# Optimization experiments

Measured on AMD Instinct MI355X. Metric: run time of the kernel, lower is better.

## Reference

```python
import jax, jax.numpy as jnp
import numpy as np

EMB = 768
HEADS = 12


def setup_inputs() -> dict:
    key = jax.random.key(0)
    ks = jax.random.split(key, 5)
    B, T, C = 4, 2048, EMB
    scale = 0.02
    return {
        "x": jax.random.normal(ks[0], (B, T, C), dtype=jnp.float32),
        "w_qkv": jax.random.normal(ks[1], (C, 3 * C), dtype=jnp.float32) * scale,
        "b_qkv": jnp.zeros((3 * C,), dtype=jnp.float32),
        "w_proj": jax.random.normal(ks[2], (C, C), dtype=jnp.float32) * scale,
        "b_proj": jnp.zeros((C,), dtype=jnp.float32),
    }


def reference(x, w_qkv, b_qkv, w_proj, b_proj):
    B, T, C = x.shape
    H = HEADS
    Dh = C // H
    qkv = x @ w_qkv + b_qkv  # [B,T,3C]
    q, k, v = jnp.split(qkv, 3, axis=-1)
    # [B,H,T,Dh]
    q = q.reshape(B, T, H, Dh).transpose(0, 2, 1, 3)
    k = k.reshape(B, T, H, Dh).transpose(0, 2, 1, 3)
    v = v.reshape(B, T, H, Dh).transpose(0, 2, 1, 3)
    scores = jnp.einsum("bhqd,bhkd->bhqk", q, k) / jnp.sqrt(jnp.float32(Dh))
    causal = jnp.tril(jnp.ones((T, T), dtype=bool))  # [T,T]
    scores = jnp.where(causal, scores, jnp.float32(-jnp.inf))
    attn = jax.nn.softmax(scores, axis=-1)
    y = jnp.einsum("bhqk,bhkd->bhqd", attn, v)  # [B,H,T,Dh]
    y = y.transpose(0, 2, 1, 3).reshape(B, T, C)
    return y @ w_proj + b_proj
```

## Files before the change

### kernel.cpp

```cpp
#include <hip/hip_runtime.h>

typedef __attribute__((ext_vector_type(8))) short short8;
typedef __attribute__((ext_vector_type(4))) float f32x4;
typedef __attribute__((ext_vector_type(4))) unsigned short ushort4v;
typedef unsigned short ushort;

__device__ __forceinline__ ushort f2bf(float f) {
    union { float f; unsigned u; } v; v.f = f;
    unsigned r = v.u + 0x7fff + ((v.u >> 16) & 1);
    return (ushort)(r >> 16);
}

__device__ __forceinline__ unsigned pkbf(float lo, float hi) {
    unsigned r;
    asm("v_cvt_pk_bf16_f32 %0, %1, %2" : "=v"(r) : "v"(lo), "v"(hi));
    return r;
}

__device__ __forceinline__ short8 bfscale8(short8 v, float s) {
    short8 o;
#pragma unroll
    for (int j = 0; j < 8; j++) {
        union { float f; unsigned u; } t; t.u = ((unsigned)(ushort)v[j]) << 16;
        o[j] = (short)f2bf(t.f * s);
    }
    return o;
}

__device__ __forceinline__ void gload16(const void* g, void* l) {
    __builtin_amdgcn_global_load_lds(
        (const __attribute__((address_space(1))) void*)g,
        (__attribute__((address_space(3))) void*)l, 16, 0, 0);
}

__global__ __launch_bounds__(256) void cvt_kernel(const float* __restrict__ in,
                                                  ushort* __restrict__ out, int n4) {
    int i = blockIdx.x * 256 + threadIdx.x;
    if (i < n4) {
        float4 v = ((const float4*)in)[i];
        ushort4v o;
        o.x = f2bf(v.x); o.y = f2bf(v.y); o.z = f2bf(v.z); o.w = f2bf(v.w);
        ((ushort4v*)out)[i] = o;
    }
}

__global__ __launch_bounds__(256) void tcvt_kernel(const float* __restrict__ in,
                                                   ushort* __restrict__ out, int R, int C0) {
    __shared__ float tile[32][33];
    const int tx = threadIdx.x & 31, ty = threadIdx.x >> 5;
    const int bx = blockIdx.x, by = blockIdx.y;
#pragma unroll
    for (int j = ty; j < 32; j += 8)
        tile[j][tx] = in[(size_t)(by * 32 + j) * C0 + bx * 32 + tx];
    __syncthreads();
#pragma unroll
    for (int j = ty; j < 32; j += 8)
        out[(size_t)(bx * 32 + j) * R + by * 32 + tx] = f2bf(tile[tx][j]);
}

__global__ __launch_bounds__(256) void vtrans_kernel(const ushort* __restrict__ qkv,
                                                     ushort* __restrict__ vt) {
    constexpr int T = 2048, H = 12, CC = 2304;
    const int bh = blockIdx.z;
    const int b = bh / H, h = bh - b * H;
    const int t0 = blockIdx.x * 32, d0 = blockIdx.y * 32;
    __shared__ ushort tile[32][33];
    const int tx = threadIdx.x & 31, ty = threadIdx.x >> 5;
#pragma unroll
    for (int j = ty; j < 32; j += 8)
        tile[j][tx] = qkv[(size_t)(b * T + t0 + j) * CC + 1536 + h * 64 + d0 + tx];
    __syncthreads();
#pragma unroll
    for (int j = ty; j < 32; j += 8)
        vt[((size_t)bh * 64 + d0 + j) * T + t0 + tx] = tile[tx][j];
}

template <bool OUT_F32>
__global__ __launch_bounds__(256)
void gemm128(const ushort* __restrict__ A, const ushort* __restrict__ Bt,
             const float* __restrict__ bias, void* __restrict__ Cout,
             int M, int N, int K) {
    __shared__ __attribute__((aligned(16))) ushort sA[2][128 * 32];
    __shared__ __attribute__((aligned(16))) ushort sB[2][128 * 32];
    const int tid = threadIdx.x;
    const int lane = tid & 63, w = tid >> 6;
    const int wm = w >> 1, wn = w & 1;
    const int c = lane & 15, g = lane >> 4;
    const int m0 = blockIdx.x * 128, n0 = blockIdx.y * 128;

    const f32x4 fz = {0.f, 0.f, 0.f, 0.f};
    f32x4 acc[4][4];
#pragma unroll
    for (int i = 0; i < 4; i++)
#pragma unroll
        for (int j = 0; j < 4; j++) acc[i][j] = fz;

    const int e0 = tid * 8, e1 = (256 + tid) * 8;
    const ushort* Ab0 = A + (size_t)(m0 + (e0 >> 5)) * K + (e0 & 31);
    const ushort* Ab1 = A + (size_t)(m0 + (e1 >> 5)) * K + (e1 & 31);
    const ushort* Bb0 = Bt + (size_t)(n0 + (e0 >> 5)) * K + (e0 & 31);
    const ushort* Bb1 = Bt + (size_t)(n0 + (e1 >> 5)) * K + (e1 & 31);

#define GSTAGE(buf, kt)                                   \
    do {                                                  \
        gload16(Ab0 + (kt) * 32, &sA[buf][e0]);           \
        gload16(Ab1 + (kt) * 32, &sA[buf][e1]);           \
        gload16(Bb0 + (kt) * 32, &sB[buf][e0]);           \
        gload16(Bb1 + (kt) * 32, &sB[buf][e1]);           \
    } while (0)

    const int nk = K >> 5;
    GSTAGE(0, 0);
    for (int kt = 0; kt < nk; ++kt) {
        __syncthreads();
        if (kt + 1 < nk) GSTAGE((kt + 1) & 1, kt + 1);
        const int cb = kt & 1;
        short8 af[4], bfr[4];
#pragma unroll
        for (int mi = 0; mi < 4; mi++)
            af[mi] = *(const short8*)&sA[cb][(wm * 64 + mi * 16 + c) * 32 + g * 8];
#pragma unroll
        for (int ni = 0; ni < 4; ni++)
            bfr[ni] = *(const short8*)&sB[cb][(wn * 64 + ni * 16 + c) * 32 + g * 8];
#pragma unroll
        for (int mi = 0; mi < 4; mi++)
#pragma unroll
            for (int ni = 0; ni < 4; ni++)
                acc[mi][ni] = __builtin_amdgcn_mfma_f32_16x16x32_bf16(
                    af[mi], bfr[ni], acc[mi][ni], 0, 0, 0);
    }
#undef GSTAGE

    const int crow = m0 + wm * 64, ccol = n0 + wn * 64;
#pragma unroll
    for (int ni = 0; ni < 4; ni++) {
        const float bv = bias[ccol + ni * 16 + c];
#pragma unroll
        for (int mi = 0; mi < 4; mi++) {
#pragma unroll
            for (int r = 0; r < 4; r++) {
                float v = acc[mi][ni][r] + bv;
                size_t idx = (size_t)(crow + mi * 16 + g * 4 + r) * N + ccol + ni * 16 + c;
                if (OUT_F32) ((float*)Cout)[idx] = v;
                else ((ushort*)Cout)[idx] = f2bf(v);
            }
        }
    }
}

__global__ __launch_bounds__(256)
void attn_fwd(const ushort* __restrict__ qkv, const ushort* __restrict__ vt,
              ushort* __restrict__ outp) {
    constexpr int T = 2048, H = 12, CC = 2304;
    const int bh = blockIdx.y;
    const int b = bh / H, h = bh - b * H;
    const int p = blockIdx.x;
    const int qt_hi = 31 - p, qt_lo = p;
    const int tid = threadIdx.x;
    const int w = tid >> 6, lane = tid & 63;
    const int c = lane & 15, g = lane >> 4;

    __shared__ __attribute__((aligned(16))) ushort sK[2][64 * 64];
    __shared__ __attribute__((aligned(16))) ushort sV[2][64 * 64];

    const int qb[2] = {qt_hi * 64 + w * 16, qt_lo * 64 + w * 16};
    const int qtl[2] = {qt_hi, qt_lo};

    const float SCL = 0.125f * 1.44269504f;
    short8 qf0[2], qf1[2];
#pragma unroll
    for (int ss = 0; ss < 2; ++ss) {
        const ushort* qp = qkv + (size_t)(b * T + qb[ss] + c) * CC + h * 64 + g * 8;
        qf0[ss] = bfscale8(*(const short8*)qp, SCL);
        qf1[ss] = bfscale8(*(const short8*)(qp + 32), SCL);
    }

    const f32x4 fz = {0.f, 0.f, 0.f, 0.f};
    f32x4 accO[2][4];
    f32x4 accL[2];
#pragma unroll
    for (int ss = 0; ss < 2; ++ss) {
        accL[ss] = fz;
#pragma unroll
        for (int ni = 0; ni < 4; ni++) accO[ss][ni] = fz;
    }

    short8 onesf;
    {
        ushort ov = (c == 0) ? (ushort)0x3F80 : (ushort)0;
#pragma unroll
        for (int j = 0; j < 8; j++) onesf[j] = (short)ov;
    }

    const int a_ = c >> 2, r_ = c & 3;
    const int rowE = 8 * a_ + r_ + 4 * (a_ & 1);
    const int rowO = 8 * a_ + r_ + 4 * ((a_ & 1) ^ 1);
    const int kaE0 = rowE * 64 + ((g ^ (rowE & 7)) << 3);
    const int kaE1 = rowE * 64 + (((4 + g) ^ (rowE & 7)) << 3);
    const int kaO0 = rowO * 64 + ((g ^ (rowO & 7)) << 3);
    const int kaO1 = rowO * 64 + (((4 + g) ^ (rowO & 7)) << 3);

    const int rowA = w * 8 + (lane >> 3);
    const int rowB = 32 + rowA;
    const int ps0 = lane & 7;
    const ushort* kS0 = qkv + (size_t)(b * T + rowA) * CC + 768 + h * 64 + ((ps0 ^ (rowA & 7)) << 3);
    const ushort* kS1 = qkv + (size_t)(b * T + rowB) * CC + 768 + h * 64 + ((ps0 ^ (rowB & 7)) << 3);
    const ushort* vS0 = vt + ((size_t)bh * 64 + rowA) * T + ((ps0 ^ (rowA & 7)) << 3);
    const ushort* vS1 = vt + ((size_t)bh * 64 + rowB) * T + ((ps0 ^ (rowB & 7)) << 3);
    const int ldK0 = (w * 8) * 64 + lane * 8;
    const int ldK1 = (32 + w * 8) * 64 + lane * 8;

#define ASTAGE(buf, kv0)                                                         \
    do {                                                                         \
        gload16(kS0 + (size_t)(kv0)*CC, &sK[buf][ldK0]);                         \
        gload16(kS1 + (size_t)(kv0)*CC, &sK[buf][ldK1]);                         \
        gload16(vS0 + (kv0), &sV[buf][ldK0]);                                    \
        gload16(vS1 + (kv0), &sV[buf][ldK1]);                                    \
    } while (0)

    ASTAGE(0, 0);
    int cur = 0;

    union U8 { unsigned u[4]; short8 s; };

    for (int t = 0; t <= qt_hi; ++t) {
        __syncthreads();
        if (t < qt_hi) ASTAGE(cur ^ 1, (t + 1) * 64);
        const ushort* K_ = &sK[cur][0];
        const ushort* V_ = &sV[cur][0];
        const bool both = (t <= qt_lo);

        f32x4 sc[2][4];
#pragma unroll
        for (int ni = 0; ni < 4; ni++) { sc[0][ni] = fz; sc[1][ni] = fz; }
#pragma unroll
        for (int ni = 0; ni < 4; ++ni) {
            const int off = (ni >> 1) * 2048;
            const int a0 = (ni & 1) ? kaO0 : kaE0;
            const int a1 = (ni & 1) ? kaO1 : kaE1;
            short8 kf0 = *(const short8*)&K_[off + a0];
            short8 kf1 = *(const short8*)&K_[off + a1];
            sc[0][ni] = __builtin_amdgcn_mfma_f32_16x16x32_bf16(kf0, qf0[0], sc[0][ni], 0, 0, 0);
            sc[0][ni] = __builtin_amdgcn_mfma_f32_16x16x32_bf16(kf1, qf1[0], sc[0][ni], 0, 0, 0);
            if (both) {
                sc[1][ni] = __builtin_amdgcn_mfma_f32_16x16x32_bf16(kf0, qf0[1], sc[1][ni], 0, 0, 0);
                sc[1][ni] = __builtin_amdgcn_mfma_f32_16x16x32_bf16(kf1, qf1[1], sc[1][ni], 0, 0, 0);
            }
        }

#pragma unroll
        for (int ss = 0; ss < 2; ++ss) {
            if (ss == 1 && !both) continue;
            if (t == qtl[ss]) {
                const int qg = qb[ss] + c;
#pragma unroll
                for (int ni = 0; ni < 4; ++ni) {
                    const int kvb = t * 64 + 8 * g + 4 * ((g & 1) ^ (ni & 1)) + 32 * (ni >> 1);
#pragma unroll
                    for (int r = 0; r < 4; ++r)
                        sc[ss][ni][r] = (kvb + r > qg) ? -1e30f : sc[ss][ni][r];
                }
            }
#pragma unroll
            for (int ni = 0; ni < 4; ++ni)
#pragma unroll
                for (int r = 0; r < 4; ++r)
                    sc[ss][ni][r] = __builtin_amdgcn_exp2f(sc[ss][ni][r]);
        }

        const bool godd = (g & 1);
#pragma unroll
        for (int ks = 0; ks < 2; ++ks) {
            short8 pf0, pf1;
            {
                f32x4 pa = godd ? sc[0][2 * ks + 1] : sc[0][2 * ks];
                f32x4 pb = godd ? sc[0][2 * ks] : sc[0][2 * ks + 1];
                U8 u;
                u.u[0] = pkbf(pa[0], pa[1]); u.u[1] = pkbf(pa[2], pa[3]);
                u.u[2] = pkbf(pb[0], pb[1]); u.u[3] = pkbf(pb[2], pb[3]);
                pf0 = u.s;
            }
            if (both) {
                f32x4 pa = godd ? sc[1][2 * ks + 1] : sc[1][2 * ks];
                f32x4 pb = godd ? sc[1][2 * ks] : sc[1][2 * ks + 1];
                U8 u;
                u.u[0] = pkbf(pa[0], pa[1]); u.u[1] = pkbf(pa[2], pa[3]);
                u.u[2] = pkbf(pb[0], pb[1]); u.u[3] = pkbf(pb[2], pb[3]);
                pf1 = u.s;
            }
#pragma unroll
            for (int ni = 0; ni < 4; ++ni) {
                short8 vf = *(const short8*)&V_[(ni * 16 + c) * 64 + (((ks * 4 + g) ^ (c & 7)) << 3)];
                accO[0][ni] = __builtin_amdgcn_mfma_f32_16x16x32_bf16(pf0, vf, accO[0][ni], 0, 0, 0);
                if (both)
                    accO[1][ni] = __builtin_amdgcn_mfma_f32_16x16x32_bf16(pf1, vf, accO[1][ni], 0, 0, 0);
            }
            accL[0] = __builtin_amdgcn_mfma_f32_16x16x32_bf16(pf0, onesf, accL[0], 0, 0, 0);
            if (both)
                accL[1] = __builtin_amdgcn_mfma_f32_16x16x32_bf16(pf1, onesf, accL[1], 0, 0, 0);
        }
        cur ^= 1;
    }
#undef ASTAGE

#pragma unroll
    for (int ss = 0; ss < 2; ++ss) {
        float linv[4];
#pragma unroll
        for (int r = 0; r < 4; r++) {
            float lv = __shfl(accL[ss][r], lane & 48, 64);
            linv[r] = 1.0f / lv;
        }
#pragma unroll
        for (int ni = 0; ni < 4; ni++)
#pragma unroll
            for (int r = 0; r < 4; r++) {
                float v = accO[ss][ni][r] * linv[r];
                outp[(size_t)(b * T + qb[ss] + g * 4 + r) * 768 + h * 64 + ni * 16 + c] = f2bf(v);
            }
    }
}

extern "C" void kernel_launch(void* const* d_in, const int* in_sizes, int n_in,
                              void* d_out, int out_size, void* d_ws, size_t ws_size,
                              hipStream_t stream) {
    const float* x      = (const float*)d_in[0];
    const float* w_qkv  = (const float*)d_in[1];
    const float* b_qkv  = (const float*)d_in[2];
    const float* w_proj = (const float*)d_in[3];
    const float* b_proj = (const float*)d_in[4];
    float* out = (float*)d_out;

    constexpr int B = 4, T = 2048, C = 768, H = 12;
    constexpr int M = B * T;
    constexpr int N1 = 3 * C;

    char* ws = (char*)d_ws;
    ushort* xb      = (ushort*)(ws);
    ushort* wqkvT   = (ushort*)(ws + 12582912);
    ushort* wprojT  = (ushort*)(ws + 16121856);
    ushort* qkvb    = (ushort*)(ws + 17301504);
    ushort* vtb     = (ushort*)(ws + 55050240);
    ushort* attnout = (ushort*)(ws + 67633152);

    cvt_kernel<<<(M * C / 4 + 255) / 256, 256, 0, stream>>>(x, xb, M * C / 4);
    tcvt_kernel<<<dim3(N1 / 32, C / 32), 256, 0, stream>>>(w_qkv, wqkvT, C, N1);
    tcvt_kernel<<<dim3(C / 32, C / 32), 256, 0, stream>>>(w_proj, wprojT, C, C);
    gemm128<false><<<dim3(M / 128, N1 / 128), 256, 0, stream>>>(xb, wqkvT, b_qkv, qkvb, M, N1, C);
    vtrans_kernel<<<dim3(T / 32, 2, B * H), 256, 0, stream>>>(qkvb, vtb);
    attn_fwd<<<dim3(16, B * H), 256, 0, stream>>>(qkvb, vtb, attnout);
    gemm128<true><<<dim3(M / 128, C / 128), 256, 0, stream>>>(attnout, wprojT, b_proj, out, M, C, C);
}
```

Measured before the change: 219.1 us.

## Fuse prep kernels, write V transposed from QKV GEMM, triple-buffer attention loads

Merges the x conversion and both weight transpose-conversions into one launch, and removes the separate V-transpose kernel by having the QKV GEMM epilogue write V columns directly into the transposed layout. The attention kernel moves from double to triple buffering of K/V tiles, using explicit vmcnt waits and raw barriers so loads run two tiles ahead, and raises wave priority around MFMA blocks. This cuts launch overhead and an extra pass over V, at the cost of more LDS per block and strided 8-byte stores in the GEMM epilogue.

```diff
diff --git a/kernel.cpp b/kernel.cpp
--- a/kernel.cpp
+++ b/kernel.cpp
@@ -33,22 +33,29 @@
         (__attribute__((address_space(3))) void*)l, 16, 0, 0);
 }
 
-__global__ __launch_bounds__(256) void cvt_kernel(const float* __restrict__ in,
-                                                  ushort* __restrict__ out, int n4) {
-    int i = blockIdx.x * 256 + threadIdx.x;
-    if (i < n4) {
-        float4 v = ((const float4*)in)[i];
+__global__ __launch_bounds__(256)
+void prep_kernel(const float* __restrict__ x, ushort* __restrict__ xb,
+                 const float* __restrict__ wq, ushort* __restrict__ wqT,
+                 const float* __restrict__ wp, ushort* __restrict__ wpT) {
+    __shared__ float tile[32][33];
+    const int bid = blockIdx.x;
+    if (bid < 6144) {
+        int i = bid * 256 + threadIdx.x;
+        float4 v = ((const float4*)x)[i];
         ushort4v o;
         o.x = f2bf(v.x); o.y = f2bf(v.y); o.z = f2bf(v.z); o.w = f2bf(v.w);
-        ((ushort4v*)out)[i] = o;
-    }
-}
-
-__global__ __launch_bounds__(256) void tcvt_kernel(const float* __restrict__ in,
-                                                   ushort* __restrict__ out, int R, int C0) {
-    __shared__ float tile[32][33];
+        ((ushort4v*)xb)[i] = o;
+        return;
+    }
+    const float* in; ushort* out; int R, C0, bx, by;
+    if (bid < 6144 + 1728) {
+        const int idx = bid - 6144;
+        in = wq; out = wqT; R = 768; C0 = 2304; bx = idx % 72; by = idx / 72;
+    } else {
+        const int idx = bid - 7872;
+        in = wp; out = wpT; R = 768; C0 = 768; bx = idx % 24; by = idx / 24;
+    }
     const int tx = threadIdx.x & 31, ty = threadIdx.x >> 5;
-    const int bx = blockIdx.x, by = blockIdx.y;
 #pragma unroll
     for (int j = ty; j < 32; j += 8)
         tile[j][tx] = in[(size_t)(by * 32 + j) * C0 + bx * 32 + tx];
@@ -58,28 +65,11 @@
         out[(size_t)(bx * 32 + j) * R + by * 32 + tx] = f2bf(tile[tx][j]);
 }
 
-__global__ __launch_bounds__(256) void vtrans_kernel(const ushort* __restrict__ qkv,
-                                                     ushort* __restrict__ vt) {
-    constexpr int T = 2048, H = 12, CC = 2304;
-    const int bh = blockIdx.z;
-    const int b = bh / H, h = bh - b * H;
-    const int t0 = blockIdx.x * 32, d0 = blockIdx.y * 32;
-    __shared__ ushort tile[32][33];
-    const int tx = threadIdx.x & 31, ty = threadIdx.x >> 5;
-#pragma unroll
-    for (int j = ty; j < 32; j += 8)
-        tile[j][tx] = qkv[(size_t)(b * T + t0 + j) * CC + 1536 + h * 64 + d0 + tx];
-    __syncthreads();
-#pragma unroll
-    for (int j = ty; j < 32; j += 8)
-        vt[((size_t)bh * 64 + d0 + j) * T + t0 + tx] = tile[tx][j];
-}
-
-template <bool OUT_F32>
+template <bool OUT_F32, bool WRITE_VT>
 __global__ __launch_bounds__(256)
 void gemm128(const ushort* __restrict__ A, const ushort* __restrict__ Bt,
              const float* __restrict__ bias, void* __restrict__ Cout,
-             int M, int N, int K) {
+             ushort* __restrict__ vt, int M, int N, int K) {
     __shared__ __attribute__((aligned(16))) ushort sA[2][128 * 32];
     __shared__ __attribute__((aligned(16))) ushort sB[2][128 * 32];
     const int tid = threadIdx.x;
@@ -135,14 +125,31 @@
 #pragma unroll
     for (int ni = 0; ni < 4; ni++) {
         const float bv = bias[ccol + ni * 16 + c];
-#pragma unroll
-        for (int mi = 0; mi < 4; mi++) {
-#pragma unroll
-            for (int r = 0; r < 4; r++) {
-                float v = acc[mi][ni][r] + bv;
-                size_t idx = (size_t)(crow + mi * 16 + g * 4 + r) * N + ccol + ni * 16 + c;
-                if (OUT_F32) ((float*)Cout)[idx] = v;
-                else ((ushort*)Cout)[idx] = f2bf(v);
+        if (WRITE_VT && (ccol + ni * 16) >= 1536) {
+            const int col = ccol + ni * 16 + c;
+            const int hv = (col - 1536) >> 6;
+            const int dv = (col - 1536) & 63;
+#pragma unroll
+            for (int mi = 0; mi < 4; mi++) {
+                const int row0 = crow + mi * 16 + g * 4;
+                const int bidx = row0 >> 11, tt = row0 & 2047;
+                ushort4v o;
+                o.x = f2bf(acc[mi][ni][0] + bv);
+                o.y = f2bf(acc[mi][ni][1] + bv);
+                o.z = f2bf(acc[mi][ni][2] + bv);
+                o.w = f2bf(acc[mi][ni][3] + bv);
+                *(ushort4v*)&vt[((size_t)(bidx * 12 + hv) * 64 + dv) * 2048 + tt] = o;
+            }
+        } else {
+#pragma unroll
+            for (int mi = 0; mi < 4; mi++) {
+#pragma unroll
+                for (int r = 0; r < 4; r++) {
+                    float v = acc[mi][ni][r] + bv;
+                    size_t idx = (size_t)(crow + mi * 16 + g * 4 + r) * N + ccol + ni * 16 + c;
+                    if (OUT_F32) ((float*)Cout)[idx] = v;
+                    else ((ushort*)Cout)[idx] = f2bf(v);
+                }
             }
         }
     }
@@ -160,8 +167,8 @@
     const int w = tid >> 6, lane = tid & 63;
     const int c = lane & 15, g = lane >> 4;
 
-    __shared__ __attribute__((aligned(16))) ushort sK[2][64 * 64];
-    __shared__ __attribute__((aligned(16))) ushort sV[2][64 * 64];
+    __shared__ __attribute__((aligned(16))) ushort sK[3][64 * 64];
+    __shared__ __attribute__((aligned(16))) ushort sV[3][64 * 64];
 
     const int qb[2] = {qt_hi * 64 + w * 16, qt_lo * 64 + w * 16};
     const int qtl[2] = {qt_hi, qt_lo};
@@ -219,13 +226,19 @@
     } while (0)
 
     ASTAGE(0, 0);
-    int cur = 0;
+    ASTAGE(1, 64);
+    int cur = 0, pfb = 2;
 
     union U8 { unsigned u[4]; short8 s; };
 
     for (int t = 0; t <= qt_hi; ++t) {
-        __syncthreads();
-        if (t < qt_hi) ASTAGE(cur ^ 1, (t + 1) * 64);
+        if (t + 1 <= qt_hi) asm volatile("s_waitcnt vmcnt(4)" ::: "memory");
+        else                asm volatile("s_waitcnt vmcnt(0)" ::: "memory");
+        __builtin_amdgcn_s_barrier();
+        asm volatile("" ::: "memory");
+        __builtin_amdgcn_sched_barrier(0);
+        if (t + 2 <= qt_hi) ASTAGE(pfb, (t + 2) * 64);
+
         const ushort* K_ = &sK[cur][0];
         const ushort* V_ = &sV[cur][0];
         const bool both = (t <= qt_lo);
@@ -233,6 +246,7 @@
         f32x4 sc[2][4];
 #pragma unroll
         for (int ni = 0; ni < 4; ni++) { sc[0][ni] = fz; sc[1][ni] = fz; }
+        __builtin_amdgcn_s_setprio(1);
 #pragma unroll
         for (int ni = 0; ni < 4; ++ni) {
             const int off = (ni >> 1) * 2048;
@@ -247,6 +261,7 @@
                 sc[1][ni] = __builtin_amdgcn_mfma_f32_16x16x32_bf16(kf1, qf1[1], sc[1][ni], 0, 0, 0);
             }
         }
+        __builtin_amdgcn_s_setprio(0);
 
 #pragma unroll
         for (int ss = 0; ss < 2; ++ss) {
@@ -288,6 +303,7 @@
                 u.u[2] = pkbf(pb[0], pb[1]); u.u[3] = pkbf(pb[2], pb[3]);
                 pf1 = u.s;
             }
+            __builtin_amdgcn_s_setprio(1);
 #pragma unroll
             for (int ni = 0; ni < 4; ++ni) {
                 short8 vf = *(const short8*)&V_[(ni * 16 + c) * 64 + (((ks * 4 + g) ^ (c & 7)) << 3)];
@@ -298,8 +314,10 @@
             accL[0] = __builtin_amdgcn_mfma_f32_16x16x32_bf16(pf0, onesf, accL[0], 0, 0, 0);
             if (both)
                 accL[1] = __builtin_amdgcn_mfma_f32_16x16x32_bf16(pf1, onesf, accL[1], 0, 0, 0);
-        }
-        cur ^= 1;
+            __builtin_amdgcn_s_setprio(0);
+        }
+        cur = (cur == 2) ? 0 : cur + 1;
+        pfb = (pfb == 2) ? 0 : pfb + 1;
     }
 #undef ASTAGE
 
@@ -343,11 +361,10 @@
     ushort* vtb     = (ushort*)(ws + 55050240);
     ushort* attnout = (ushort*)(ws + 67633152);
 
-    cvt_kernel<<<(M * C / 4 + 255) / 256, 256, 0, stream>>>(x, xb, M * C / 4);
-    tcvt_kernel<<<dim3(N1 / 32, C / 32), 256, 0, stream>>>(w_qkv, wqkvT, C, N1);
-    tcvt_kernel<<<dim3(C / 32, C / 32), 256, 0, stream>>>(w_proj, wprojT, C, C);
-    gemm128<false><<<dim3(M / 128, N1 / 128), 256, 0, stream>>>(xb, wqkvT, b_qkv, qkvb, M, N1, C);
-    vtrans_kernel<<<dim3(T / 32, 2, B * H), 256, 0, stream>>>(qkvb, vtb);
+    prep_kernel<<<8448, 256, 0, stream>>>(x, xb, w_qkv, wqkvT, w_proj, wprojT);
+    gemm128<false, true><<<dim3(M / 128, N1 / 128), 256, 0, stream>>>(
+        xb, wqkvT, b_qkv, qkvb, vtb, M, N1, C);
     attn_fwd<<<dim3(16, B * H), 256, 0, stream>>>(qkvb, vtb, attnout);
-    gemm128<true><<<dim3(M / 128, C / 128), 256, 0, stream>>>(attnout, wprojT, b_proj, out, M, C, C);
-}
+    gemm128<true, false><<<dim3(M / 128, C / 128), 256, 0, stream>>>(
+        attnout, wprojT, b_proj, out, nullptr, M, C, C);
+}
```

Result: faster. 210.2 us (-4.0%).
